# Performance work log

Hardware: AMD Instinct MI355X
Metric: run time of the kernel (lower is better)

The kernel has to match this reference:

```python
import jax, jax.numpy as jnp
import numpy as np

VOCAB_SIZE = 4096
D_EMBED = 256
BETA = 0.25  # unused: module returns raw commit_loss; beta applied by caller


def setup_inputs() -> dict:
    key = jax.random.key(0)
    k_h, k_e = jax.random.split(key)
    h = jax.random.normal(k_h, (16, D_EMBED, 32, 32), dtype=jnp.float32)
    embedding = jax.random.normal(k_e, (VOCAB_SIZE, D_EMBED), dtype=jnp.float32)
    return {"h": h, "embedding": embedding}


def reference(h, embedding):
    B, C, H, W = h.shape
    h = h.astype(jnp.float32)
    # (B, C, H, W) -> (N, C) with N = B*H*W
    h_flat = jnp.transpose(h, (0, 2, 3, 1)).reshape(-1, C)
    dist = (
        jnp.sum(h_flat * h_flat, axis=1, keepdims=True)
        + jnp.sum(embedding * embedding, axis=1)
        - 2.0 * jnp.einsum("nc,vc->nv", h_flat, embedding)
    )
    indices_flat = jnp.argmin(dist, axis=1)
    indices = indices_flat.reshape(B, H, W)
    # gather codebook vectors and restore (B, C, H, W)
    z_q = jnp.transpose(embedding[indices_flat].reshape(B, H, W, C), (0, 3, 1, 2))
    commit_loss = jnp.mean((h - jax.lax.stop_gradient(z_q)) ** 2)
    # straight-through estimator
    z_q_st = h + jax.lax.stop_gradient(z_q - h)
    return z_q_st, indices, commit_loss
```

## Files before the change

### kernel.cpp

```cpp
#include <hip/hip_runtime.h>

#define D 256
#define VOCAB 4096
#define NTOT 16384
#define N_OUT0 4194304

typedef _Float16 half8 __attribute__((ext_vector_type(8)));
typedef float f32x4 __attribute__((ext_vector_type(4)));

__device__ __forceinline__ void gld16(const void* g, void* l) {
    __builtin_amdgcn_global_load_lds(
        (const __attribute__((address_space(1))) void*)g,
        (__attribute__((address_space(3))) void*)l, 16, 0, 0);
}

__device__ __forceinline__ unsigned long long pack_key(float d, int v) {
    unsigned u = __float_as_uint(d);
    u ^= ((unsigned)((int)u >> 31)) | 0x80000000u;
    return ((unsigned long long)u << 32) | (unsigned)v;
}

__global__ __launch_bounds__(64) void k_prep(const float* __restrict__ emb,
                                             float* __restrict__ esq,
                                             unsigned long long* __restrict__ gbest,
                                             float* __restrict__ out2) {
    const int v = blockIdx.x, lane = threadIdx.x;
    float4 e = *(const float4*)(emb + (size_t)v * D + lane * 4);
    float s = e.x * e.x + e.y * e.y + e.z * e.z + e.w * e.w;
#pragma unroll
    for (int m = 32; m >= 1; m >>= 1) s += __shfl_xor(s, m, 64);
    if (lane == 0) esq[v] = s;
    if (v < NTOT / 64) gbest[(size_t)v * 64 + lane] = ~0ULL;
    if (v == 0 && lane == 0) out2[0] = 0.0f;
}

__global__ __launch_bounds__(256) void k_pack(const float* __restrict__ h,
                                              const float* __restrict__ emb,
                                              _Float16* __restrict__ Apk,
                                              _Float16* __restrict__ Bpk) {
    __shared__ float S[8192];
    const int tid = threadIdx.x;
    const int bid = blockIdx.x;
    if (bid < 512) {
        const int bm = bid >> 3, w = bid & 7;
        const int b = bm >> 2, p0 = (bm & 3) * 256;
        const float* src = h + ((size_t)b << 18) + p0;
#pragma unroll 4
        for (int cl = 0; cl < 32; ++cl)
            S[cl * 256 + tid] = src[(size_t)(w * 32 + cl) << 10 | (unsigned)tid];
        __syncthreads();
        _Float16* dstT = Apk + (size_t)bm * 131072 + (size_t)w * 16384;
#pragma unroll
        for (int i = 0; i < 4; ++i) {
            alignas(16) _Float16 hi[8], lo[8];
#pragma unroll
            for (int j = 0; j < 8; ++j) {
                float vv = S[(i * 8 + j) * 256 + tid];
                _Float16 hv = (_Float16)vv;
                hi[j] = hv;
                lo[j] = (_Float16)(vv - (float)hv);
            }
            _Float16* dst = dstT + i * 2048 + tid * 8;
            *(half8*)dst = *(half8*)hi;
            *(half8*)(dst + 8192) = *(half8*)lo;
        }
    } else {
        const int bid2 = bid - 512;
        const int bn = bid2 >> 3, w = bid2 & 7;
        const int v0 = bn * 128;
#pragma unroll 4
        for (int i = 0; i < 16; ++i) {
            int flat = i * 256 + tid;
            int r = flat >> 5, cl = flat & 31;
            S[cl * 129 + r] = emb[(size_t)(v0 + r) * D + w * 32 + cl];
        }
        __syncthreads();
        _Float16* dstT = Bpk + (size_t)bn * 65536 + (size_t)w * 8192;
#pragma unroll
        for (int i = 0; i < 2; ++i) {
            int s = i * 256 + tid;
            int q = s >> 7, r = s & 127;
            alignas(16) _Float16 hi[8], lo[8];
#pragma unroll
            for (int j = 0; j < 8; ++j) {
                float vv = S[(q * 8 + j) * 129 + r];
                _Float16 hv = (_Float16)vv;
                hi[j] = hv;
                lo[j] = (_Float16)(vv - (float)hv);
            }
            _Float16* dst = dstT + q * 1024 + r * 8;
            *(half8*)dst = *(half8*)hi;
            *(half8*)(dst + 4096) = *(half8*)lo;
        }
    }
}

__global__ __launch_bounds__(256, 2) void k_gemm(const _Float16* __restrict__ Apk,
                                                 const _Float16* __restrict__ Bpk,
                                                 const float* __restrict__ esq,
                                                 unsigned long long* __restrict__ gbest) {
    __shared__ _Float16 As[16384];
    __shared__ _Float16 Bs[8192];
    __shared__ unsigned long long red[256];

    const int tid = threadIdx.x;
    const int bm = blockIdx.x >> 5, bn = blockIdx.x & 31;
    const int m0 = bm * 256, n0 = bn * 128;
    red[tid] = ~0ULL;

    const int wv = tid >> 6, l = tid & 63;
    const int wm = wv & 1, wn = wv >> 1;
    const int quad = l >> 4, j16 = l & 15;

    f32x4 acc[8][4];
#pragma unroll
    for (int i = 0; i < 8; ++i)
#pragma unroll
        for (int j = 0; j < 4; ++j) acc[i][j] = (f32x4)0.0f;

    const _Float16* Aw0 = Apk + (size_t)bm * 131072;
    const _Float16* Bw0 = Bpk + (size_t)bn * 65536;
    const _Float16* aBase = As + quad * 2048 + (wm * 128 + j16) * 8;
    const _Float16* bBase = Bs + quad * 1024 + (wn * 64 + j16) * 8;

    for (int w = 0; w < 8; ++w) {
        const _Float16* Aw = Aw0 + w * 16384;
        const _Float16* Bw = Bw0 + w * 8192;
#pragma unroll
        for (int i = 0; i < 8; ++i) gld16(Aw + i * 2048 + tid * 8, As + i * 2048 + tid * 8);
#pragma unroll
        for (int i = 0; i < 4; ++i) gld16(Bw + i * 2048 + tid * 8, Bs + i * 2048 + tid * 8);
        __syncthreads();

        half8 af[8], bf[4];
#pragma unroll
        for (int mt = 0; mt < 8; ++mt) af[mt] = *(const half8*)(aBase + mt * 128);
#pragma unroll
        for (int nt = 0; nt < 4; ++nt) bf[nt] = *(const half8*)(bBase + 4096 + nt * 128);
#pragma unroll
        for (int mt = 0; mt < 8; ++mt)
#pragma unroll
            for (int nt = 0; nt < 4; ++nt)
                acc[mt][nt] = __builtin_amdgcn_mfma_f32_16x16x32_f16(af[mt], bf[nt], acc[mt][nt], 0, 0, 0);
#pragma unroll
        for (int nt = 0; nt < 4; ++nt) bf[nt] = *(const half8*)(bBase + nt * 128);
#pragma unroll
        for (int mt = 0; mt < 8; ++mt)
#pragma unroll
            for (int nt = 0; nt < 4; ++nt)
                acc[mt][nt] = __builtin_amdgcn_mfma_f32_16x16x32_f16(af[mt], bf[nt], acc[mt][nt], 0, 0, 0);
#pragma unroll
        for (int mt = 0; mt < 8; ++mt) af[mt] = *(const half8*)(aBase + 8192 + mt * 128);
#pragma unroll
        for (int mt = 0; mt < 8; ++mt)
#pragma unroll
            for (int nt = 0; nt < 4; ++nt)
                acc[mt][nt] = __builtin_amdgcn_mfma_f32_16x16x32_f16(af[mt], bf[nt], acc[mt][nt], 0, 0, 0);
        __syncthreads();
    }

    float es[4];
#pragma unroll
    for (int nt = 0; nt < 4; ++nt) es[nt] = esq[n0 + wn * 64 + nt * 16 + j16];
#pragma unroll
    for (int mt = 0; mt < 8; ++mt) {
#pragma unroll
        for (int r = 0; r < 4; ++r) {
            unsigned long long best = ~0ULL;
#pragma unroll
            for (int nt = 0; nt < 4; ++nt) {
                float dv = es[nt] - 2.0f * acc[mt][nt][r];
                unsigned long long key = pack_key(dv, n0 + wn * 64 + nt * 16 + j16);
                best = key < best ? key : best;
            }
#pragma unroll
            for (int m = 8; m >= 1; m >>= 1) {
                unsigned long long o = __shfl_xor(best, m, 64);
                best = o < best ? o : best;
            }
            if (j16 == 0) atomicMin(&red[wm * 128 + mt * 16 + quad * 4 + r], best);
        }
    }
    __syncthreads();
    atomicMin(&gbest[m0 + tid], red[tid]);
}

__global__ __launch_bounds__(256) void k_gather(const float* __restrict__ h,
                                                const float* __restrict__ emb,
                                                const unsigned long long* __restrict__ gbest,
                                                float* __restrict__ out0,
                                                float* __restrict__ out1,
                                                float* __restrict__ out2) {
    __shared__ float zq[32][260];
    __shared__ float wred[4];
    const int tid = threadIdx.x;
    const int lane = tid & 63;
    const int w = tid >> 6;
    const int n0 = blockIdx.x * 32;
    const int b = n0 >> 10;
    const int p0 = n0 & 1023;
#pragma unroll
    for (int rr = 0; rr < 8; ++rr) {
        int r = w * 8 + rr;
        unsigned idx = (unsigned)(gbest[n0 + r] & 0xFFFFFFFFULL);
        float4 e4 = *(const float4*)(emb + (size_t)idx * D + lane * 4);
        *(float4*)&zq[r][lane * 4] = e4;
    }
    if (tid < 32) {
        unsigned idx = (unsigned)(gbest[n0 + tid] & 0xFFFFFFFFULL);
        out1[n0 + tid] = (float)idx;
    }
    __syncthreads();
    float lsum = 0.0f;
    const size_t base = ((size_t)b * D) << 10;
#pragma unroll 4
    for (int it = 0; it < 32; ++it) {
        int c = it * 8 + (tid >> 5);
        int pp = tid & 31;
        float z = zq[pp][c];
        size_t g = base + ((size_t)c << 10) + p0 + pp;
        float hv = h[g];
        out0[g] = hv + (z - hv);
        float d = hv - z;
        lsum = fmaf(d, d, lsum);
    }
#pragma unroll
    for (int m = 32; m >= 1; m >>= 1) lsum += __shfl_xor(lsum, m, 64);
    if (lane == 0) wred[w] = lsum;
    __syncthreads();
    if (tid == 0)
        atomicAdd(out2, (wred[0] + wred[1] + wred[2] + wred[3]) * (1.0f / (float)N_OUT0));
}

extern "C" void kernel_launch(void* const* d_in, const int* in_sizes, int n_in,
                              void* d_out, int out_size, void* d_ws, size_t ws_size,
                              hipStream_t stream) {
    const float* h = (const float*)d_in[0];
    const float* emb = (const float*)d_in[1];
    float* out0 = (float*)d_out;
    float* out1 = out0 + N_OUT0;
    float* out2 = out1 + NTOT;

    _Float16* Apk = (_Float16*)d_ws;
    _Float16* Bpk = (_Float16*)((char*)d_ws + 16777216);
    float* esq = (float*)((char*)d_ws + 16777216 + 4194304);
    unsigned long long* gbest = (unsigned long long*)((char*)d_ws + 16777216 + 4194304 + 16384);

    hipLaunchKernelGGL(k_prep, dim3(VOCAB), dim3(64), 0, stream, emb, esq, gbest, out2);
    hipLaunchKernelGGL(k_pack, dim3(768), dim3(256), 0, stream, h, emb, Apk, Bpk);
    hipLaunchKernelGGL(k_gemm, dim3(2048), dim3(256), 0, stream, Apk, Bpk, esq, gbest);
    hipLaunchKernelGGL(k_gather, dim3(NTOT / 32), dim3(256), 0, stream, h, emb, gbest, out0, out1, out2);
}
```

Before: 194.3 us.

## Double-buffer LDS in distance GEMM with 256x256 tiles and 8 waves

Restructures the distance GEMM to use 512-thread blocks on 256x256 output tiles. LDS is now double-buffered: the next K-slice is staged with async global-to-LDS loads while MFMAs run on the current slice, using explicit vmcnt waits and barriers per phase. The change also adds block-index swizzling for L2 locality and raises MFMA wave priority. The goal is to hide global-load latency and halve B-tile refetch, at the cost of more LDS (128KB per block) and fragile hand-tuned wait counts.

After: 199.2 us. 2.5% more time.

```diff
diff --git a/kernel.cpp b/kernel.cpp
--- a/kernel.cpp
+++ b/kernel.cpp
@@ -95,22 +95,69 @@
     }
 }
 
-__global__ __launch_bounds__(256, 2) void k_gemm(const _Float16* __restrict__ Apk,
+
+#define STAGE_A_HI(W, NB) do { const _Float16* s_ = Ag + (W) * 16384; \
+    gld16(s_ + tid * 8, As + (NB) + tid * 8); \
+    gld16(s_ + 4096 + tid * 8, As + (NB) + 4096 + tid * 8); } while (0)
+#define STAGE_A_LO(W, NB) do { const _Float16* s_ = Ag + (W) * 16384 + 8192; \
+    gld16(s_ + tid * 8, As + (NB) + 8192 + tid * 8); \
+    gld16(s_ + 4096 + tid * 8, As + (NB) + 12288 + tid * 8); } while (0)
+#define STAGE_B_LO(W, NB) do { \
+    gld16(Bg0 + (W) * 8192 + 4096 + tid * 8, Bs + (NB) + 4096 + tid * 8); \
+    gld16(Bg1 + (W) * 8192 + 4096 + tid * 8, Bs + (NB) + 12288 + tid * 8); } while (0)
+#define STAGE_B_HI(W, NB) do { \
+    gld16(Bg0 + (W) * 8192 + tid * 8, Bs + (NB) + tid * 8); \
+    gld16(Bg1 + (W) * 8192 + tid * 8, Bs + (NB) + 8192 + tid * 8); } while (0)
+
+#define LOAD_AF(OFF) do { _Pragma("unroll") \
+    for (int mt_ = 0; mt_ < 8; ++mt_) af[mt_] = *(const half8*)(aB + (OFF) + mt_ * 128); } while (0)
+#define LOAD_BF(OFF) do { _Pragma("unroll") \
+    for (int nt_ = 0; nt_ < 4; ++nt_) bf[nt_] = *(const half8*)(bB + (OFF) + nt_ * 128); } while (0)
+
+#define MFMA32() do { \
+    __builtin_amdgcn_s_setprio(1); \
+    _Pragma("unroll") \
+    for (int mt_ = 0; mt_ < 8; ++mt_) { \
+      _Pragma("unroll") \
+      for (int nt_ = 0; nt_ < 4; ++nt_) \
+        acc[mt_][nt_] = __builtin_amdgcn_mfma_f32_16x16x32_f16(af[mt_], bf[nt_], acc[mt_][nt_], 0, 0, 0); \
+    } \
+    __builtin_amdgcn_s_setprio(0); \
+  } while (0)
+
+#define PHASE_END(N) do { \
+    __builtin_amdgcn_sched_barrier(0); \
+    asm volatile("s_waitcnt vmcnt(" #N ")" ::: "memory"); \
+    __builtin_amdgcn_s_barrier(); } while (0)
+
+__global__ __launch_bounds__(512, 2) void k_gemm(const _Float16* __restrict__ Apk,
                                                  const _Float16* __restrict__ Bpk,
                                                  const float* __restrict__ esq,
                                                  unsigned long long* __restrict__ gbest) {
-    __shared__ _Float16 As[16384];
-    __shared__ _Float16 Bs[8192];
-    __shared__ unsigned long long red[256];
+    __shared__ alignas(16) _Float16 As[32768];
+    __shared__ alignas(16) _Float16 Bs[32768];
 
     const int tid = threadIdx.x;
-    const int bm = blockIdx.x >> 5, bn = blockIdx.x & 31;
-    const int m0 = bm * 256, n0 = bn * 128;
-    red[tid] = ~0ULL;
+    const int bid = blockIdx.x;
+    const int swz = (bid & 7) * 128 + (bid >> 3);
+    const int bm = swz >> 4, bn = swz & 15;
+    const int m0 = bm * 256, n0 = bn * 256;
+
+    const _Float16* Ag = Apk + (size_t)bm * 131072;
+    const _Float16* Bg0 = Bpk + (size_t)(2 * bn) * 65536;
+    const _Float16* Bg1 = Bpk + (size_t)(2 * bn + 1) * 65536;
+
+    STAGE_A_HI(0, 0);
+    STAGE_B_LO(0, 0);
+    STAGE_B_HI(0, 0);
+    STAGE_A_LO(0, 0);
 
     const int wv = tid >> 6, l = tid & 63;
     const int wm = wv & 1, wn = wv >> 1;
     const int quad = l >> 4, j16 = l & 15;
+    const int arow = wm * 128 + j16;
+    const int brow = (wn & 1) * 64 + j16;
+    const int bsub = wn >> 1;
 
     f32x4 acc[8][4];
 #pragma unroll
@@ -118,46 +165,58 @@
 #pragma unroll
         for (int j = 0; j < 4; ++j) acc[i][j] = (f32x4)0.0f;
 
-    const _Float16* Aw0 = Apk + (size_t)bm * 131072;
-    const _Float16* Bw0 = Bpk + (size_t)bn * 65536;
-    const _Float16* aBase = As + quad * 2048 + (wm * 128 + j16) * 8;
-    const _Float16* bBase = Bs + quad * 1024 + (wn * 64 + j16) * 8;
-
-    for (int w = 0; w < 8; ++w) {
-        const _Float16* Aw = Aw0 + w * 16384;
-        const _Float16* Bw = Bw0 + w * 8192;
-#pragma unroll
-        for (int i = 0; i < 8; ++i) gld16(Aw + i * 2048 + tid * 8, As + i * 2048 + tid * 8);
-#pragma unroll
-        for (int i = 0; i < 4; ++i) gld16(Bw + i * 2048 + tid * 8, Bs + i * 2048 + tid * 8);
-        __syncthreads();
-
+    asm volatile("s_waitcnt vmcnt(4)" ::: "memory");
+    __builtin_amdgcn_s_barrier();
+
+#pragma unroll 1
+    for (int w = 0; w < 7; ++w) {
+        const int cb = (w & 1) << 14, nb = cb ^ 16384;
+        const _Float16* aB = As + cb + quad * 2048 + arow * 8;
+        const _Float16* bB = Bs + cb + bsub * 8192 + quad * 1024 + brow * 8;
         half8 af[8], bf[4];
-#pragma unroll
-        for (int mt = 0; mt < 8; ++mt) af[mt] = *(const half8*)(aBase + mt * 128);
-#pragma unroll
-        for (int nt = 0; nt < 4; ++nt) bf[nt] = *(const half8*)(bBase + 4096 + nt * 128);
-#pragma unroll
-        for (int mt = 0; mt < 8; ++mt)
-#pragma unroll
-            for (int nt = 0; nt < 4; ++nt)
-                acc[mt][nt] = __builtin_amdgcn_mfma_f32_16x16x32_f16(af[mt], bf[nt], acc[mt][nt], 0, 0, 0);
-#pragma unroll
-        for (int nt = 0; nt < 4; ++nt) bf[nt] = *(const half8*)(bBase + nt * 128);
-#pragma unroll
-        for (int mt = 0; mt < 8; ++mt)
-#pragma unroll
-            for (int nt = 0; nt < 4; ++nt)
-                acc[mt][nt] = __builtin_amdgcn_mfma_f32_16x16x32_f16(af[mt], bf[nt], acc[mt][nt], 0, 0, 0);
-#pragma unroll
-        for (int mt = 0; mt < 8; ++mt) af[mt] = *(const half8*)(aBase + 8192 + mt * 128);
-#pragma unroll
-        for (int mt = 0; mt < 8; ++mt)
-#pragma unroll
-            for (int nt = 0; nt < 4; ++nt)
-                acc[mt][nt] = __builtin_amdgcn_mfma_f32_16x16x32_f16(af[mt], bf[nt], acc[mt][nt], 0, 0, 0);
-        __syncthreads();
-    }
+
+        LOAD_AF(0);
+        LOAD_BF(4096);
+        STAGE_A_HI(w + 1, nb);
+        STAGE_B_LO(w + 1, nb);
+        __builtin_amdgcn_s_barrier();
+        MFMA32();
+        PHASE_END(6);
+
+        LOAD_BF(0);
+        STAGE_B_HI(w + 1, nb);
+        __builtin_amdgcn_s_barrier();
+        MFMA32();
+        PHASE_END(6);
+
+        LOAD_AF(8192);
+        STAGE_A_LO(w + 1, nb);
+        __builtin_amdgcn_s_barrier();
+        MFMA32();
+        PHASE_END(4);
+    }
+    {
+        const _Float16* aB = As + 16384 + quad * 2048 + arow * 8;
+        const _Float16* bB = Bs + 16384 + bsub * 8192 + quad * 1024 + brow * 8;
+        half8 af[8], bf[4];
+        LOAD_AF(0);
+        LOAD_BF(4096);
+        __builtin_amdgcn_s_barrier();
+        MFMA32();
+        PHASE_END(2);
+        LOAD_BF(0);
+        __builtin_amdgcn_s_barrier();
+        MFMA32();
+        PHASE_END(0);
+        LOAD_AF(8192);
+        __builtin_amdgcn_s_barrier();
+        MFMA32();
+    }
+
+    unsigned long long* red = (unsigned long long*)As;
+    __syncthreads();
+    if (tid < 256) red[tid] = ~0ULL;
+    __syncthreads();
 
     float es[4];
 #pragma unroll
@@ -182,7 +241,7 @@
         }
     }
     __syncthreads();
-    atomicMin(&gbest[m0 + tid], red[tid]);
+    if (tid < 256) atomicMin(&gbest[m0 + tid], red[tid]);
 }
 
 __global__ __launch_bounds__(256) void k_gather(const float* __restrict__ h,
@@ -248,6 +307,6 @@
 
     hipLaunchKernelGGL(k_prep, dim3(VOCAB), dim3(64), 0, stream, emb, esq, gbest, out2);
     hipLaunchKernelGGL(k_pack, dim3(768), dim3(256), 0, stream, h, emb, Apk, Bpk);
-    hipLaunchKernelGGL(k_gemm, dim3(2048), dim3(256), 0, stream, Apk, Bpk, esq, gbest);
+    hipLaunchKernelGGL(k_gemm, dim3(1024), dim3(512), 0, stream, Apk, Bpk, esq, gbest);
     hipLaunchKernelGGL(k_gather, dim3(NTOT / 32), dim3(256), 0, stream, h, emb, gbest, out0, out1, out2);
 }
```
